# Kernel tuning notes

Measured on AMD Instinct MI355X. Metric: run time of the kernel, lower is better.

The kernel has to match this reference:

```python
import jax, jax.numpy as jnp
import numpy as np

N_NODES = 100000
N_EDGES = 1600000
IN_FEATS = 64
OUT_FEATS = 64
BN_EPS = 1e-5


def setup_inputs() -> dict:
    key = jax.random.key(0)
    ks = jax.random.split(key, 5)
    feats = jax.random.normal(ks[0], (N_NODES, IN_FEATS), dtype=jnp.float32)
    src = jax.random.randint(ks[1], (N_EDGES,), 0, N_NODES, dtype=jnp.int32)
    dst = jax.random.randint(ks[2], (N_EDGES,), 0, N_NODES, dtype=jnp.int32)
    scale = 1.0 / np.sqrt(IN_FEATS)
    W = jax.random.normal(ks[3], (IN_FEATS, OUT_FEATS), dtype=jnp.float32) * scale
    b = jnp.zeros((OUT_FEATS,), dtype=jnp.float32)
    Wr = jax.random.normal(ks[4], (IN_FEATS, OUT_FEATS), dtype=jnp.float32) * scale
    br = jnp.zeros((OUT_FEATS,), dtype=jnp.float32)
    gamma = jnp.ones((OUT_FEATS,), dtype=jnp.float32)
    beta = jnp.zeros((OUT_FEATS,), dtype=jnp.float32)
    return {"feats": feats, "src": src, "dst": dst, "W": W, "b": b,
            "Wr": Wr, "br": br, "gamma": gamma, "beta": beta}


def reference(feats, src, dst, W, b, Wr, br, gamma, beta):
    N = feats.shape[0]
    # GraphConv(norm='none'): sum-aggregate source features into destinations (SpMM),
    # then linear + bias + activation (relu).
    agg = jax.ops.segment_sum(feats[src], dst, num_segments=N)  # [N, IN]
    h = jax.nn.relu(agg @ W + b)                                # [N, OUT]
    # residual branch: activation(Linear(feats))
    res = jax.nn.relu(feats @ Wr + br)
    h = h + res
    # dropout p=0.0 -> identity
    # BatchNorm1d (training mode): biased variance over node dim, eps=1e-5
    mean = jnp.mean(h, axis=0)
    var = jnp.var(h, axis=0)
    return (h - mean) * jax.lax.rsqrt(var + BN_EPS) * gamma + beta
```

## Files before the change

kernel.cpp:

```cpp
#include <hip/hip_runtime.h>
#include <hip/hip_bf16.h>


typedef __attribute__((ext_vector_type(8))) short short8;
typedef __attribute__((ext_vector_type(4))) float f32x4;

constexpr int BKT  = 64;
constexpr int NBKT_MAX = 2048;
constexpr int SCAP = 1536;
constexpr int PB   = 8192;
constexpr int CAST_BLKS = 800;

static __device__ __forceinline__ float bfbits_lo(unsigned u) {
    union { unsigned u; float f; } c; c.u = u << 16; return c.f;
}
static __device__ __forceinline__ float bfbits_hi(unsigned u) {
    union { unsigned u; float f; } c; c.u = u & 0xffff0000u; return c.f;
}
static __device__ __forceinline__ short bf16r(float x) {
    __hip_bfloat16 h = __float2bfloat16(x);
    union { __hip_bfloat16 h; short s; } c; c.h = h; return c.s;
}
static __device__ __forceinline__ unsigned bf16pair(float x, float y) {
    return (unsigned)(unsigned short)bf16r(x) | ((unsigned)(unsigned short)bf16r(y) << 16);
}

__global__ __launch_bounds__(1024) void k_prep_part(
    const int* __restrict__ src, const int* __restrict__ dst,
    int* __restrict__ cursor, unsigned* __restrict__ pk_slots,
    int n_edges, int nbatch, int nbkt,
    const float* __restrict__ feats, unsigned short* __restrict__ feats_h, int total8,
    const float* __restrict__ W, const float* __restrict__ Wr,
    short* __restrict__ Wpk, short* __restrict__ Wrpk)
{
    __shared__ int hist[NBKT_MAX], basei[NBKT_MAX], cnt2[NBKT_MAX];
    const int bid = blockIdx.x;
    const int tid = threadIdx.x;
    if (bid < nbatch) {
        const int e0 = bid * PB;
        for (int i = tid; i < nbkt; i += 1024) { hist[i] = 0; cnt2[i] = 0; }
        __syncthreads();
        unsigned pk[8]; unsigned short bb8[8];
        #pragma unroll
        for (int i = 0; i < 8; i++) {
            const int e = e0 + i * 1024 + tid;
            if (e < n_edges) {
                const int d = dst[e];
                const int s = src[e];
                const int bb = d >> 6;
                bb8[i] = (unsigned short)bb;
                pk[i] = ((unsigned)(d & 63) << 17) | (unsigned)s;
                atomicAdd(&hist[bb], 1);
            } else bb8[i] = 0xffff;
        }
        __syncthreads();
        for (int i = tid; i < nbkt; i += 1024) {
            const int c = hist[i];
            basei[i] = (c > 0) ? atomicAdd(&cursor[i], c) : 0;
        }
        __syncthreads();
        #pragma unroll
        for (int i = 0; i < 8; i++) {
            if (bb8[i] != 0xffff) {
                const int bb = bb8[i];
                const int pos = basei[bb] + atomicAdd(&cnt2[bb], 1);
                if (pos < SCAP)
                    pk_slots[(size_t)bb * SCAP + pos] = pk[i];
            }
        }
    } else if (bid < nbatch + CAST_BLKS) {
        const int cb = bid - nbatch;
        for (int i = cb * 1024 + tid; i < total8; i += CAST_BLKS * 1024) {
            float4 v0 = ((const float4*)feats)[i * 2];
            float4 v1 = ((const float4*)feats)[i * 2 + 1];
            short8 o;
            o[0] = bf16r(v0.x); o[1] = bf16r(v0.y); o[2] = bf16r(v0.z); o[3] = bf16r(v0.w);
            o[4] = bf16r(v1.x); o[5] = bf16r(v1.y); o[6] = bf16r(v1.z); o[7] = bf16r(v1.w);
            ((short8*)feats_h)[i] = o;
        }
    } else {
        for (int idx = tid; idx < 8192; idx += 1024) {
            const int m = idx >> 12;
            const int rem = idx & 4095;
            const int j = rem & 7;
            const int q = rem >> 3;
            const int lane = q & 63;
            const int st = q >> 6;
            const int s = st >> 2;
            const int t = st & 3;
            const int k = s * 32 + (lane >> 4) * 8 + j;
            const int n = t * 16 + (lane & 15);
            const float v = (m == 0) ? W[k * 64 + n] : Wr[k * 64 + n];
            short* out = (m == 0) ? Wpk : Wrpk;
            out[rem] = bf16r(v);
        }
    }
}

__global__ __launch_bounds__(512) void k_gsort(
    const unsigned short* __restrict__ feats_h, const int* __restrict__ cursor,
    const unsigned* __restrict__ pk_slots, unsigned short* __restrict__ aggh,
    int n_nodes)
{
    __shared__ unsigned raw[SCAP];
    __shared__ unsigned srt[SCAP];
    __shared__ int cnt[BKT], cnt2[BKT], lofs[BKT], noff[BKT + 1];
    const int bkt = blockIdx.x;
    const int tid = threadIdx.x;
    int m = cursor[bkt]; if (m > SCAP) m = SCAP;
    const unsigned* gsl = pk_slots + (size_t)bkt * SCAP;

    if (tid < BKT) { cnt[tid] = 0; cnt2[tid] = 0; }
    __syncthreads();
    for (int i = tid; i < m; i += 512) {
        const unsigned p = gsl[i];
        raw[i] = p;
        atomicAdd(&cnt[p >> 17], 1);
    }
    __syncthreads();
    if (tid < BKT) lofs[tid] = cnt[tid];
    __syncthreads();
    for (int off = 1; off < BKT; off <<= 1) {
        int x = 0;
        if (tid < BKT && tid >= off) x = lofs[tid - off];
        __syncthreads();
        if (tid < BKT) lofs[tid] += x;
        __syncthreads();
    }
    if (tid < BKT) noff[tid + 1] = lofs[tid];
    if (tid == 0) noff[0] = 0;
    __syncthreads();
    for (int i = tid; i < m; i += 512) {
        const unsigned p = raw[i];
        const int d = p >> 17;
        srt[noff[d] + atomicAdd(&cnt2[d], 1)] = p & 0x1ffffu;
    }
    __syncthreads();

    const int wave = tid >> 6;
    const int lane = tid & 63;
    const int half = lane >> 5;
    const int li   = lane & 31;
    #pragma unroll 1
    for (int k = 0; k < 8; k++) {
        const int nl = wave * 8 + k;
        const int n  = bkt * BKT + nl;
        if (n >= n_nodes) break;
        const int beg = noff[nl], end = noff[nl + 1];
        float ax[4] = {0.f, 0.f, 0.f, 0.f};
        float ay[4] = {0.f, 0.f, 0.f, 0.f};
        int base = beg;
        for (; base + 16 <= end; base += 16) {
            #pragma unroll
            for (int j = 0; j < 8; j++) {
                const unsigned s = srt[base + 2 * j + half];
                const unsigned v = *(const unsigned*)(feats_h + (size_t)s * 64 + li * 2);
                ax[j & 3] += bfbits_lo(v);
                ay[j & 3] += bfbits_hi(v);
            }
        }
        if (base < end) {
            #pragma unroll
            for (int j = 0; j < 8; j++) {
                const int e = base + 2 * j + half;
                const bool vd = e < end;
                const unsigned s = srt[vd ? e : beg];
                const unsigned v = *(const unsigned*)(feats_h + (size_t)s * 64 + li * 2);
                ax[j & 3] += vd ? bfbits_lo(v) : 0.f;
                ay[j & 3] += vd ? bfbits_hi(v) : 0.f;
            }
        }
        float axs = (ax[0] + ax[1]) + (ax[2] + ax[3]);
        float ays = (ay[0] + ay[1]) + (ay[2] + ay[3]);
        axs += __shfl_xor(axs, 32);
        ays += __shfl_xor(ays, 32);
        if (half == 0)
            *(unsigned*)(aggh + (size_t)n * 128 + li * 2) = bf16pair(axs, ays);
    }
}

__global__ __launch_bounds__(512) void k_mv(
    const unsigned short* aggh, const unsigned short* __restrict__ feats_h,
    const short* __restrict__ Wpk, const short* __restrict__ Wrpk,
    const float* __restrict__ b, const float* __restrict__ br,
    float* h, float* __restrict__ bnacc, int n_nodes)
{
    __shared__ float ssum[64], ssq[64];
    const int tid = threadIdx.x;
    const int wave = tid >> 6;
    const int lane = tid & 63;
    if (tid < 64) { ssum[tid] = 0.f; ssq[tid] = 0.f; }
    __syncthreads();

    short8 wf[8], wrf[8];
    #pragma unroll
    for (int i = 0; i < 8; i++) {
        wf[i]  = *(const short8*)(Wpk  + (i * 64 + lane) * 8);
        wrf[i] = *(const short8*)(Wrpk + (i * 64 + lane) * 8);
    }
    float bt[4], brt[4];
    #pragma unroll
    for (int t = 0; t < 4; t++) {
        bt[t]  = b [t * 16 + (lane & 15)];
        brt[t] = br[t * 16 + (lane & 15)];
    }

    const int r0 = blockIdx.x * 128 + wave * 16;
    int arow = r0 + (lane & 15);
    if (arow >= n_nodes) arow = n_nodes - 1;
    const int kb = (lane >> 4) * 8;

    short8 aggA[2], feaA[2];
    #pragma unroll
    for (int s = 0; s < 2; s++) {
        aggA[s] = *(const short8*)(aggh + (size_t)arow * 128 + s * 32 + kb);
        feaA[s] = *(const short8*)(feats_h + (size_t)arow * 64 + s * 32 + kb);
    }

    #pragma unroll
    for (int t = 0; t < 4; t++) {
        f32x4 c1 = {0.f, 0.f, 0.f, 0.f};
        f32x4 c2 = {0.f, 0.f, 0.f, 0.f};
        c1 = __builtin_amdgcn_mfma_f32_16x16x32_bf16(aggA[0], wf [t],     c1, 0, 0, 0);
        c1 = __builtin_amdgcn_mfma_f32_16x16x32_bf16(aggA[1], wf [4 + t], c1, 0, 0, 0);
        c2 = __builtin_amdgcn_mfma_f32_16x16x32_bf16(feaA[0], wrf[t],     c2, 0, 0, 0);
        c2 = __builtin_amdgcn_mfma_f32_16x16x32_bf16(feaA[1], wrf[4 + t], c2, 0, 0, 0);
        const int col = t * 16 + (lane & 15);
        float ls = 0.f, lq = 0.f;
        #pragma unroll
        for (int r = 0; r < 4; r++) {
            const int row = r0 + (lane >> 4) * 4 + r;
            const float hv = fmaxf(c1[r] + bt[t], 0.f) + fmaxf(c2[r] + brt[t], 0.f);
            if (row < n_nodes) {
                h[(size_t)row * 64 + col] = hv;
                ls += hv;
                lq += hv * hv;
            }
        }
        ls += __shfl_xor(ls, 16); ls += __shfl_xor(ls, 32);
        lq += __shfl_xor(lq, 16); lq += __shfl_xor(lq, 32);
        if ((lane >> 4) == 0) {
            atomicAdd(&ssum[col], ls);
            atomicAdd(&ssq[col], lq);
        }
    }
    __syncthreads();
    if (tid < 64) {
        atomicAdd(&bnacc[tid], ssum[tid]);
        atomicAdd(&bnacc[64 + tid], ssq[tid]);
    }
}

__global__ __launch_bounds__(256) void k_bnapply(
    float* __restrict__ h, const float* __restrict__ bnacc,
    const float* __restrict__ gamma, const float* __restrict__ beta,
    int total4, float inv_n)
{
    __shared__ float ssc[64], ssh[64];
    if (threadIdx.x < 64) {
        const int t = threadIdx.x;
        const float mean = bnacc[t] * inv_n;
        const float var  = bnacc[64 + t] * inv_n - mean * mean;
        const float sc = gamma[t] * rsqrtf(var + 1e-5f);
        ssc[t] = sc;
        ssh[t] = beta[t] - mean * sc;
    }
    __syncthreads();
    for (int i = blockIdx.x * blockDim.x + threadIdx.x; i < total4;
         i += gridDim.x * blockDim.x) {
        float4 v = ((float4*)h)[i];
        const int j = (i & 15) << 2;
        v.x = v.x * ssc[j + 0] + ssh[j + 0];
        v.y = v.y * ssc[j + 1] + ssh[j + 1];
        v.z = v.z * ssc[j + 2] + ssh[j + 2];
        v.w = v.w * ssc[j + 3] + ssh[j + 3];
        ((float4*)h)[i] = v;
    }
}

extern "C" void kernel_launch(void* const* d_in, const int* in_sizes, int n_in,
                              void* d_out, int out_size, void* d_ws, size_t ws_size,
                              hipStream_t stream)
{
    const float* feats = (const float*)d_in[0];
    const int*   src   = (const int*)  d_in[1];
    const int*   dst   = (const int*)  d_in[2];
    const float* W     = (const float*)d_in[3];
    const float* b     = (const float*)d_in[4];
    const float* Wr    = (const float*)d_in[5];
    const float* br    = (const float*)d_in[6];
    const float* gamma = (const float*)d_in[7];
    const float* beta  = (const float*)d_in[8];

    const int n_nodes = in_sizes[0] / 64;
    const int n_edges = in_sizes[1];
    const int nbkt    = (n_nodes + BKT - 1) / BKT;
    const int nbatch  = (n_edges + PB - 1) / PB;

    int*      cursor   = (int*)d_ws;
    float*    bnacc    = (float*)(cursor + NBKT_MAX);
    unsigned* pk_slots = (unsigned*)(bnacc + 128);
    unsigned short* feats_h = (unsigned short*)(pk_slots + (size_t)nbkt * SCAP);
    short*    Wpk      = (short*)(feats_h + (size_t)n_nodes * 64);
    short*    Wrpk     = Wpk + 4096;
    unsigned short* aggh = (unsigned short*)d_out;
    float*    h        = (float*)d_out;

    hipMemsetAsync(cursor, 0, (size_t)(NBKT_MAX + 128) * sizeof(int), stream);

    k_prep_part<<<nbatch + CAST_BLKS + 1, 1024, 0, stream>>>(
        src, dst, cursor, pk_slots, n_edges, nbatch, nbkt,
        feats, feats_h, n_nodes * 8, W, Wr, Wpk, Wrpk);
    k_gsort<<<nbkt, 512, 0, stream>>>(feats_h, cursor, pk_slots, aggh, n_nodes);
    k_mv   <<<(n_nodes + 127) / 128, 512, 0, stream>>>(aggh, feats_h, Wpk, Wrpk,
                                                       b, br, h, bnacc, n_nodes);
    k_bnapply<<<2048, 256, 0, stream>>>(h, bnacc, gamma, beta, n_nodes * 16,
                                        1.f / (float)n_nodes);
}
```

Before: 103.2 us.

## Split bucket cursors and slots per XCD to localize global atomics

The partition kernel now reads the hardware XCC id and keeps a separate cursor and slot region per bucket for each XCD. This is meant to cut cross-die atomic contention and cache-line ping-pong on the shared cursors. The sort kernel gathers the eight per-XCD segments and swaps its shared-memory scan for a wavefront shuffle scan. The per-XCD capacity of 192 can drop edges if the distribution is skewed, and the memset grows eightfold.

```diff
diff --git a/kernel.cpp b/kernel.cpp
--- a/kernel.cpp
+++ b/kernel.cpp
@@ -7,10 +7,16 @@
 
 constexpr int BKT  = 64;
 constexpr int NBKT_MAX = 2048;
+constexpr int LCAP = 192;
 constexpr int SCAP = 1536;
 constexpr int PB   = 8192;
 constexpr int CAST_BLKS = 800;
 
+static __device__ __forceinline__ int xcc_id() {
+    int x;
+    asm volatile("s_getreg_b32 %0, hwreg(HW_REG_XCC_ID)" : "=s"(x));
+    return x & 7;
+}
 static __device__ __forceinline__ float bfbits_lo(unsigned u) {
     union { unsigned u; float f; } c; c.u = u << 16; return c.f;
 }
@@ -37,6 +43,7 @@
     const int bid = blockIdx.x;
     const int tid = threadIdx.x;
     if (bid < nbatch) {
+        const int xcd = xcc_id();
         const int e0 = bid * PB;
         for (int i = tid; i < nbkt; i += 1024) { hist[i] = 0; cnt2[i] = 0; }
         __syncthreads();
@@ -56,7 +63,7 @@
         __syncthreads();
         for (int i = tid; i < nbkt; i += 1024) {
             const int c = hist[i];
-            basei[i] = (c > 0) ? atomicAdd(&cursor[i], c) : 0;
+            basei[i] = (c > 0) ? atomicAdd(&cursor[i * 8 + xcd], c) : 0;
         }
         __syncthreads();
         #pragma unroll
@@ -64,8 +71,8 @@
             if (bb8[i] != 0xffff) {
                 const int bb = bb8[i];
                 const int pos = basei[bb] + atomicAdd(&cnt2[bb], 1);
-                if (pos < SCAP)
-                    pk_slots[(size_t)bb * SCAP + pos] = pk[i];
+                if (pos < LCAP)
+                    pk_slots[((size_t)bb * 8 + xcd) * LCAP + pos] = pk[i];
             }
         }
     } else if (bid < nbatch + CAST_BLKS) {
@@ -104,32 +111,49 @@
 {
     __shared__ unsigned raw[SCAP];
     __shared__ unsigned srt[SCAP];
-    __shared__ int cnt[BKT], cnt2[BKT], lofs[BKT], noff[BKT + 1];
+    __shared__ int cnt[BKT], cnt2[BKT], noff[BKT + 1];
     const int bkt = blockIdx.x;
     const int tid = threadIdx.x;
-    int m = cursor[bkt]; if (m > SCAP) m = SCAP;
-    const unsigned* gsl = pk_slots + (size_t)bkt * SCAP;
+    const unsigned* lanebase = pk_slots + (size_t)bkt * 8 * LCAP;
 
     if (tid < BKT) { cnt[tid] = 0; cnt2[tid] = 0; }
     __syncthreads();
-    for (int i = tid; i < m; i += 512) {
-        const unsigned p = gsl[i];
-        raw[i] = p;
-        atomicAdd(&cnt[p >> 17], 1);
-    }
-    __syncthreads();
-    if (tid < BKT) lofs[tid] = cnt[tid];
-    __syncthreads();
-    for (int off = 1; off < BKT; off <<= 1) {
-        int x = 0;
-        if (tid < BKT && tid >= off) x = lofs[tid - off];
-        __syncthreads();
-        if (tid < BKT) lofs[tid] += x;
-        __syncthreads();
-    }
-    if (tid < BKT) noff[tid + 1] = lofs[tid];
-    if (tid == 0) noff[0] = 0;
-    __syncthreads();
+
+    int segoff[9];
+    segoff[0] = 0;
+    #pragma unroll
+    for (int x = 0; x < 8; x++) {
+        int c = cursor[bkt * 8 + x];
+        c = c > LCAP ? LCAP : c;
+        const int room = SCAP - segoff[x];
+        c = c > room ? room : c;
+        segoff[x + 1] = segoff[x] + c;
+    }
+    #pragma unroll 1
+    for (int x = 0; x < 8; x++) {
+        const int c = segoff[x + 1] - segoff[x];
+        const unsigned* gp = lanebase + (size_t)x * LCAP;
+        for (int i = tid; i < c; i += 512) {
+            const unsigned p = gp[i];
+            raw[segoff[x] + i] = p;
+            atomicAdd(&cnt[p >> 17], 1);
+        }
+    }
+    const int m = segoff[8];
+    __syncthreads();
+
+    if (tid < 64) {
+        int v = cnt[tid];
+        #pragma unroll
+        for (int off = 1; off < 64; off <<= 1) {
+            const int y = __shfl_up(v, off);
+            if (tid >= off) v += y;
+        }
+        noff[tid + 1] = v;
+        if (tid == 0) noff[0] = 0;
+    }
+    __syncthreads();
+
     for (int i = tid; i < m; i += 512) {
         const unsigned p = raw[i];
         const int d = p >> 17;
@@ -298,15 +322,15 @@
     const int nbatch  = (n_edges + PB - 1) / PB;
 
     int*      cursor   = (int*)d_ws;
-    float*    bnacc    = (float*)(cursor + NBKT_MAX);
+    float*    bnacc    = (float*)(cursor + (size_t)NBKT_MAX * 8);
     unsigned* pk_slots = (unsigned*)(bnacc + 128);
-    unsigned short* feats_h = (unsigned short*)(pk_slots + (size_t)nbkt * SCAP);
+    unsigned short* feats_h = (unsigned short*)(pk_slots + (size_t)nbkt * 8 * LCAP);
     short*    Wpk      = (short*)(feats_h + (size_t)n_nodes * 64);
     short*    Wrpk     = Wpk + 4096;
     unsigned short* aggh = (unsigned short*)d_out;
     float*    h        = (float*)d_out;
 
-    hipMemsetAsync(cursor, 0, (size_t)(NBKT_MAX + 128) * sizeof(int), stream);
+    hipMemsetAsync(cursor, 0, ((size_t)NBKT_MAX * 8 + 128) * sizeof(int), stream);
 
     k_prep_part<<<nbatch + CAST_BLKS + 1, 1024, 0, stream>>>(
         src, dst, cursor, pk_slots, n_edges, nbatch, nbkt,
```

After: 108.4 us. +5.0%, slower.

## Fuse gather-aggregate with MFMA linear stage and enlarge edge partition batches

Applied to the files above, without the earlier changes.

Merges the gather/sort aggregation kernel with the MFMA matmul kernel, so each 64-node bucket's aggregated bf16 rows stay in LDS instead of going through global memory. This removes one kernel launch and a global write/read of the aggregate. The edge partition batch grows from 8192 to 32768 edges per block, which cuts global cursor atomics but gives fewer, longer blocks. Other changes: the gather now uses 8-byte loads with four edges in flight per wave, the in-bucket scan uses wave shuffles, and dst/src are re-read instead of held in registers. Only half the waves do the MFMA stage, which may leave the block underused there.

```diff
diff --git a/kernel.cpp b/kernel.cpp
--- a/kernel.cpp
+++ b/kernel.cpp
@@ -8,7 +8,7 @@
 constexpr int BKT  = 64;
 constexpr int NBKT_MAX = 2048;
 constexpr int SCAP = 1536;
-constexpr int PB   = 8192;
+constexpr int PB   = 32768;
 constexpr int CAST_BLKS = 800;
 
 static __device__ __forceinline__ float bfbits_lo(unsigned u) {
@@ -38,35 +38,25 @@
     const int tid = threadIdx.x;
     if (bid < nbatch) {
         const int e0 = bid * PB;
+        const int e1 = (e0 + PB < n_edges) ? e0 + PB : n_edges;
         for (int i = tid; i < nbkt; i += 1024) { hist[i] = 0; cnt2[i] = 0; }
         __syncthreads();
-        unsigned pk[8]; unsigned short bb8[8];
-        #pragma unroll
-        for (int i = 0; i < 8; i++) {
-            const int e = e0 + i * 1024 + tid;
-            if (e < n_edges) {
-                const int d = dst[e];
-                const int s = src[e];
-                const int bb = d >> 6;
-                bb8[i] = (unsigned short)bb;
-                pk[i] = ((unsigned)(d & 63) << 17) | (unsigned)s;
-                atomicAdd(&hist[bb], 1);
-            } else bb8[i] = 0xffff;
-        }
+        for (int e = e0 + tid; e < e1; e += 1024)
+            atomicAdd(&hist[dst[e] >> 6], 1);
         __syncthreads();
         for (int i = tid; i < nbkt; i += 1024) {
             const int c = hist[i];
             basei[i] = (c > 0) ? atomicAdd(&cursor[i], c) : 0;
         }
         __syncthreads();
-        #pragma unroll
-        for (int i = 0; i < 8; i++) {
-            if (bb8[i] != 0xffff) {
-                const int bb = bb8[i];
-                const int pos = basei[bb] + atomicAdd(&cnt2[bb], 1);
-                if (pos < SCAP)
-                    pk_slots[(size_t)bb * SCAP + pos] = pk[i];
-            }
+        for (int e = e0 + tid; e < e1; e += 1024) {
+            const int d = dst[e];
+            const int s = src[e];
+            const int bb = d >> 6;
+            const int pos = basei[bb] + atomicAdd(&cnt2[bb], 1);
+            if (pos < SCAP)
+                pk_slots[(size_t)bb * SCAP + pos] =
+                    ((unsigned)(d & 63) << 17) | (unsigned)s;
         }
     } else if (bid < nbatch + CAST_BLKS) {
         const int cb = bid - nbatch;
@@ -97,41 +87,42 @@
     }
 }
 
-__global__ __launch_bounds__(512) void k_gsort(
+__global__ __launch_bounds__(512) void k_gmv(
     const unsigned short* __restrict__ feats_h, const int* __restrict__ cursor,
-    const unsigned* __restrict__ pk_slots, unsigned short* __restrict__ aggh,
-    int n_nodes)
+    const unsigned* __restrict__ pk_slots,
+    const short* __restrict__ Wpk, const short* __restrict__ Wrpk,
+    const float* __restrict__ b, const float* __restrict__ br,
+    float* __restrict__ h, float* __restrict__ bnacc, int n_nodes)
 {
-    __shared__ unsigned raw[SCAP];
     __shared__ unsigned srt[SCAP];
-    __shared__ int cnt[BKT], cnt2[BKT], lofs[BKT], noff[BKT + 1];
+    __shared__ short aggL[64 * 72];
+    __shared__ int cnt[BKT], cnt2[BKT], noff[BKT + 1];
+    __shared__ float ssum[64], ssq[64];
     const int bkt = blockIdx.x;
     const int tid = threadIdx.x;
     int m = cursor[bkt]; if (m > SCAP) m = SCAP;
     const unsigned* gsl = pk_slots + (size_t)bkt * SCAP;
 
     if (tid < BKT) { cnt[tid] = 0; cnt2[tid] = 0; }
+    if (tid < 64)  { ssum[tid] = 0.f; ssq[tid] = 0.f; }
+    __syncthreads();
+
+    for (int i = tid; i < m; i += 512)
+        atomicAdd(&cnt[gsl[i] >> 17], 1);
+    __syncthreads();
+    if (tid < 64) {
+        int v = cnt[tid];
+        #pragma unroll
+        for (int off = 1; off < 64; off <<= 1) {
+            const int y = __shfl_up(v, off);
+            if (tid >= off) v += y;
+        }
+        noff[tid + 1] = v;
+        if (tid == 0) noff[0] = 0;
+    }
     __syncthreads();
     for (int i = tid; i < m; i += 512) {
         const unsigned p = gsl[i];
-        raw[i] = p;
-        atomicAdd(&cnt[p >> 17], 1);
-    }
-    __syncthreads();
-    if (tid < BKT) lofs[tid] = cnt[tid];
-    __syncthreads();
-    for (int off = 1; off < BKT; off <<= 1) {
-        int x = 0;
-        if (tid < BKT && tid >= off) x = lofs[tid - off];
-        __syncthreads();
-        if (tid < BKT) lofs[tid] += x;
-        __syncthreads();
-    }
-    if (tid < BKT) noff[tid + 1] = lofs[tid];
-    if (tid == 0) noff[0] = 0;
-    __syncthreads();
-    for (int i = tid; i < m; i += 512) {
-        const unsigned p = raw[i];
         const int d = p >> 17;
         srt[noff[d] + atomicAdd(&cnt2[d], 1)] = p & 0x1ffffu;
     }
@@ -139,109 +130,102 @@
 
     const int wave = tid >> 6;
     const int lane = tid & 63;
-    const int half = lane >> 5;
-    const int li   = lane & 31;
+    const int slot = lane >> 4;
+    const int q    = lane & 15;
     #pragma unroll 1
     for (int k = 0; k < 8; k++) {
         const int nl = wave * 8 + k;
         const int n  = bkt * BKT + nl;
         if (n >= n_nodes) break;
         const int beg = noff[nl], end = noff[nl + 1];
-        float ax[4] = {0.f, 0.f, 0.f, 0.f};
-        float ay[4] = {0.f, 0.f, 0.f, 0.f};
+        float a0 = 0.f, a1 = 0.f, a2 = 0.f, a3 = 0.f;
         int base = beg;
         for (; base + 16 <= end; base += 16) {
             #pragma unroll
-            for (int j = 0; j < 8; j++) {
-                const unsigned s = srt[base + 2 * j + half];
-                const unsigned v = *(const unsigned*)(feats_h + (size_t)s * 64 + li * 2);
-                ax[j & 3] += bfbits_lo(v);
-                ay[j & 3] += bfbits_hi(v);
+            for (int g = 0; g < 4; g++) {
+                const unsigned s = srt[base + 4 * g + slot];
+                const uint2 v = *(const uint2*)(feats_h + (size_t)s * 64 + q * 4);
+                a0 += bfbits_lo(v.x); a1 += bfbits_hi(v.x);
+                a2 += bfbits_lo(v.y); a3 += bfbits_hi(v.y);
             }
         }
         if (base < end) {
             #pragma unroll
-            for (int j = 0; j < 8; j++) {
-                const int e = base + 2 * j + half;
+            for (int g = 0; g < 4; g++) {
+                const int e = base + 4 * g + slot;
                 const bool vd = e < end;
                 const unsigned s = srt[vd ? e : beg];
-                const unsigned v = *(const unsigned*)(feats_h + (size_t)s * 64 + li * 2);
-                ax[j & 3] += vd ? bfbits_lo(v) : 0.f;
-                ay[j & 3] += vd ? bfbits_hi(v) : 0.f;
+                const uint2 v = *(const uint2*)(feats_h + (size_t)s * 64 + q * 4);
+                a0 += vd ? bfbits_lo(v.x) : 0.f;
+                a1 += vd ? bfbits_hi(v.x) : 0.f;
+                a2 += vd ? bfbits_lo(v.y) : 0.f;
+                a3 += vd ? bfbits_hi(v.y) : 0.f;
             }
         }
-        float axs = (ax[0] + ax[1]) + (ax[2] + ax[3]);
-        float ays = (ay[0] + ay[1]) + (ay[2] + ay[3]);
-        axs += __shfl_xor(axs, 32);
-        ays += __shfl_xor(ays, 32);
-        if (half == 0)
-            *(unsigned*)(aggh + (size_t)n * 128 + li * 2) = bf16pair(axs, ays);
-    }
-}
-
-__global__ __launch_bounds__(512) void k_mv(
-    const unsigned short* aggh, const unsigned short* __restrict__ feats_h,
-    const short* __restrict__ Wpk, const short* __restrict__ Wrpk,
-    const float* __restrict__ b, const float* __restrict__ br,
-    float* h, float* __restrict__ bnacc, int n_nodes)
-{
-    __shared__ float ssum[64], ssq[64];
-    const int tid = threadIdx.x;
-    const int wave = tid >> 6;
-    const int lane = tid & 63;
-    if (tid < 64) { ssum[tid] = 0.f; ssq[tid] = 0.f; }
-    __syncthreads();
-
-    short8 wf[8], wrf[8];
-    #pragma unroll
-    for (int i = 0; i < 8; i++) {
-        wf[i]  = *(const short8*)(Wpk  + (i * 64 + lane) * 8);
-        wrf[i] = *(const short8*)(Wrpk + (i * 64 + lane) * 8);
-    }
-    float bt[4], brt[4];
-    #pragma unroll
-    for (int t = 0; t < 4; t++) {
-        bt[t]  = b [t * 16 + (lane & 15)];
-        brt[t] = br[t * 16 + (lane & 15)];
-    }
-
-    const int r0 = blockIdx.x * 128 + wave * 16;
-    int arow = r0 + (lane & 15);
-    if (arow >= n_nodes) arow = n_nodes - 1;
-    const int kb = (lane >> 4) * 8;
-
-    short8 aggA[2], feaA[2];
-    #pragma unroll
-    for (int s = 0; s < 2; s++) {
-        aggA[s] = *(const short8*)(aggh + (size_t)arow * 128 + s * 32 + kb);
-        feaA[s] = *(const short8*)(feats_h + (size_t)arow * 64 + s * 32 + kb);
-    }
-
-    #pragma unroll
-    for (int t = 0; t < 4; t++) {
-        f32x4 c1 = {0.f, 0.f, 0.f, 0.f};
-        f32x4 c2 = {0.f, 0.f, 0.f, 0.f};
-        c1 = __builtin_amdgcn_mfma_f32_16x16x32_bf16(aggA[0], wf [t],     c1, 0, 0, 0);
-        c1 = __builtin_amdgcn_mfma_f32_16x16x32_bf16(aggA[1], wf [4 + t], c1, 0, 0, 0);
-        c2 = __builtin_amdgcn_mfma_f32_16x16x32_bf16(feaA[0], wrf[t],     c2, 0, 0, 0);
-        c2 = __builtin_amdgcn_mfma_f32_16x16x32_bf16(feaA[1], wrf[4 + t], c2, 0, 0, 0);
-        const int col = t * 16 + (lane & 15);
-        float ls = 0.f, lq = 0.f;
-        #pragma unroll
-        for (int r = 0; r < 4; r++) {
-            const int row = r0 + (lane >> 4) * 4 + r;
-            const float hv = fmaxf(c1[r] + bt[t], 0.f) + fmaxf(c2[r] + brt[t], 0.f);
-            if (row < n_nodes) {
-                h[(size_t)row * 64 + col] = hv;
-                ls += hv;
-                lq += hv * hv;
+        a0 += __shfl_xor(a0, 16); a0 += __shfl_xor(a0, 32);
+        a1 += __shfl_xor(a1, 16); a1 += __shfl_xor(a1, 32);
+        a2 += __shfl_xor(a2, 16); a2 += __shfl_xor(a2, 32);
+        a3 += __shfl_xor(a3, 16); a3 += __shfl_xor(a3, 32);
+        if (slot == 0) {
+            uint2 o;
+            o.x = bf16pair(a0, a1);
+            o.y = bf16pair(a2, a3);
+            *(uint2*)(&aggL[nl * 72 + q * 4]) = o;
+        }
+    }
+    __syncthreads();
+
+    if (wave < 4) {
+        short8 wf[8], wrf[8];
+        #pragma unroll
+        for (int i = 0; i < 8; i++) {
+            wf[i]  = *(const short8*)(Wpk  + (i * 64 + lane) * 8);
+            wrf[i] = *(const short8*)(Wrpk + (i * 64 + lane) * 8);
+        }
+        float bt[4], brt[4];
+        #pragma unroll
+        for (int t = 0; t < 4; t++) {
+            bt[t]  = b [t * 16 + (lane & 15)];
+            brt[t] = br[t * 16 + (lane & 15)];
+        }
+        const int rl0 = wave * 16;
+        const int arow_l = rl0 + (lane & 15);
+        const int kb = (lane >> 4) * 8;
+        int grow = bkt * BKT + arow_l;
+        if (grow >= n_nodes) grow = n_nodes - 1;
+
+        short8 aggA[2], feaA[2];
+        #pragma unroll
+        for (int s = 0; s < 2; s++) {
+            aggA[s] = *(const short8*)(&aggL[arow_l * 72 + s * 32 + kb]);
+            feaA[s] = *(const short8*)(feats_h + (size_t)grow * 64 + s * 32 + kb);
+        }
+        #pragma unroll
+        for (int t = 0; t < 4; t++) {
+            f32x4 c1 = {0.f, 0.f, 0.f, 0.f};
+            f32x4 c2 = {0.f, 0.f, 0.f, 0.f};
+            c1 = __builtin_amdgcn_mfma_f32_16x16x32_bf16(aggA[0], wf [t],     c1, 0, 0, 0);
+            c1 = __builtin_amdgcn_mfma_f32_16x16x32_bf16(aggA[1], wf [4 + t], c1, 0, 0, 0);
+            c2 = __builtin_amdgcn_mfma_f32_16x16x32_bf16(feaA[0], wrf[t],     c2, 0, 0, 0);
+            c2 = __builtin_amdgcn_mfma_f32_16x16x32_bf16(feaA[1], wrf[4 + t], c2, 0, 0, 0);
+            const int col = t * 16 + (lane & 15);
+            float ls = 0.f, lq = 0.f;
+            #pragma unroll
+            for (int r = 0; r < 4; r++) {
+                const int row = bkt * BKT + rl0 + (lane >> 4) * 4 + r;
+                const float hv = fmaxf(c1[r] + bt[t], 0.f) + fmaxf(c2[r] + brt[t], 0.f);
+                if (row < n_nodes) {
+                    h[(size_t)row * 64 + col] = hv;
+                    ls += hv;
+                    lq += hv * hv;
+                }
             }
-        }
-        ls += __shfl_xor(ls, 16); ls += __shfl_xor(ls, 32);
-        lq += __shfl_xor(lq, 16); lq += __shfl_xor(lq, 32);
-        if ((lane >> 4) == 0) {
-            atomicAdd(&ssum[col], ls);
-            atomicAdd(&ssq[col], lq);
+            ls += __shfl_xor(ls, 16); ls += __shfl_xor(ls, 32);
+            lq += __shfl_xor(lq, 16); lq += __shfl_xor(lq, 32);
+            if ((lane >> 4) == 0) {
+                atomicAdd(&ssum[col], ls);
+                atomicAdd(&ssq[col], lq);
+            }
         }
     }
     __syncthreads();
@@ -303,7 +287,6 @@
     unsigned short* feats_h = (unsigned short*)(pk_slots + (size_t)nbkt * SCAP);
     short*    Wpk      = (short*)(feats_h + (size_t)n_nodes * 64);
     short*    Wrpk     = Wpk + 4096;
-    unsigned short* aggh = (unsigned short*)d_out;
     float*    h        = (float*)d_out;
 
     hipMemsetAsync(cursor, 0, (size_t)(NBKT_MAX + 128) * sizeof(int), stream);
@@ -311,9 +294,8 @@
     k_prep_part<<<nbatch + CAST_BLKS + 1, 1024, 0, stream>>>(
         src, dst, cursor, pk_slots, n_edges, nbatch, nbkt,
         feats, feats_h, n_nodes * 8, W, Wr, Wpk, Wrpk);
-    k_gsort<<<nbkt, 512, 0, stream>>>(feats_h, cursor, pk_slots, aggh, n_nodes);
-    k_mv   <<<(n_nodes + 127) / 128, 512, 0, stream>>>(aggh, feats_h, Wpk, Wrpk,
-                                                       b, br, h, bnacc, n_nodes);
+    k_gmv<<<nbkt, 512, 0, stream>>>(feats_h, cursor, pk_slots, Wpk, Wrpk,
+                                    b, br, h, bnacc, n_nodes);
     k_bnapply<<<2048, 256, 0, stream>>>(h, bnacc, gamma, beta, n_nodes * 16,
                                         1.f / (float)n_nodes);
 }
```

Result: slower. 137.1 us (+32.9%).
